# Optimization experiments

Measured on AMD Instinct MI355X. Metric: run time of the kernel, lower is better.

The kernel has to match this reference:

```python
import jax, jax.numpy as jnp
import numpy as np

D_PAIR = 128
D_BIAS = 128
N_HEAD = 4
D_HID = 32
B = 1
L = 384
EPS = 1e-5


def _layernorm(x, gamma, beta):
    m = jnp.mean(x, axis=-1, keepdims=True)
    v = jnp.var(x, axis=-1, keepdims=True)
    return (x - m) * jax.lax.rsqrt(v + EPS) * gamma + beta


def setup_inputs() -> dict:
    key = jax.random.key(0)
    ks = jax.random.split(key, 10)
    hd = N_HEAD * D_HID
    s = 0.02
    return {
        "pair": jax.random.normal(ks[0], (B, L, L, D_PAIR), jnp.float32),
        "bias": jax.random.normal(ks[1], (B, L, L, D_BIAS), jnp.float32),
        "gamma_p": jnp.ones((D_PAIR,), jnp.float32),
        "beta_p": jnp.zeros((D_PAIR,), jnp.float32),
        "gamma_b": jnp.ones((D_BIAS,), jnp.float32),
        "beta_b": jnp.zeros((D_BIAS,), jnp.float32),
        "Wq": jax.random.normal(ks[2], (D_PAIR, hd), jnp.float32) * s,
        "Wk": jax.random.normal(ks[3], (D_PAIR, hd), jnp.float32) * s,
        "Wv": jax.random.normal(ks[4], (D_PAIR, hd), jnp.float32) * s,
        "Wb": jax.random.normal(ks[5], (D_BIAS, N_HEAD), jnp.float32) * s,
        "Wg": jax.random.normal(ks[6], (D_PAIR, hd), jnp.float32) * s,
        "bg": jnp.ones((hd,), jnp.float32),
        "Wout": jax.random.normal(ks[7], (hd, D_PAIR), jnp.float32) * s,
        "bout": jnp.zeros((D_PAIR,), jnp.float32),
    }


def reference(pair, bias, gamma_p, beta_p, gamma_b, beta_b,
              Wq, Wk, Wv, Wb, Wg, bg, Wout, bout):
    h = Wb.shape[1]
    d = Wq.shape[1] // h
    Bn, Ln = pair.shape[:2]
    scaling = 1.0 / jnp.sqrt(jnp.asarray(d, pair.dtype))

    # is_row=True: attend along rows -> swap the two L axes
    pair_t = jnp.transpose(pair, (0, 2, 1, 3))
    bias_t = jnp.transpose(bias, (0, 2, 1, 3))

    pn = _layernorm(pair_t, gamma_p, beta_p)                     # [B,L,L,dp]
    q = (pn @ Wq).reshape(Bn, Ln, Ln, h, d) * scaling            # [B,n,i,h,d]
    k = (pn @ Wk).reshape(Bn, Ln, Ln, h, d) / Ln                 # [B,n,j,h,d]

    # mean-over-n biased axial attention logits: [B,i,j,h]
    attn = jnp.einsum('bnihk,bnjhk->bijh', q, k)
    attn = attn + _layernorm(bias_t, gamma_b, beta_b) @ Wb       # learned bias
    a = jax.nn.softmax(attn, axis=-2)                            # over j

    v = (pn @ Wv).reshape(Bn, Ln, Ln, h, d)                      # [B,n,j,h,d]
    o = jnp.einsum('bijh,bnjhd->bnihd', a, v).reshape(Bn, Ln, Ln, h * d)

    gate = jax.nn.sigmoid(pn @ Wg + bg)                          # [B,L,L,h*d]
    out = (gate * o) @ Wout + bout                               # [B,L,L,dp]

    return jnp.transpose(out, (0, 2, 1, 3))                      # undo is_row permute
```

## Files before the change

kernel.cpp:

```cpp
#include <hip/hip_runtime.h>

typedef unsigned short u16;
typedef unsigned int   u32;
typedef __attribute__((ext_vector_type(8))) short bf16x8;
typedef __attribute__((ext_vector_type(4))) float f32x4;

#define LL 384
#define DP 128
#define SZROW ((size_t)LL * LL)

#define SWZ(row, col) (((row) << 7) + (((((col) >> 3) ^ ((row) & 7)) << 3) | ((col) & 7)))

__device__ __forceinline__ u16 f2bf(float x) {
  u32 u = __builtin_bit_cast(u32, x);
  u = (u + 0x7FFFu + ((u >> 16) & 1u)) >> 16;
  return (u16)u;
}
__device__ __forceinline__ float bf2f(u16 h) {
  return __builtin_bit_cast(float, ((u32)h) << 16);
}
__device__ __forceinline__ uint2 pack4(float a, float b, float c, float d) {
  uint2 p;
  p.x = (u32)f2bf(a) | ((u32)f2bf(b) << 16);
  p.y = (u32)f2bf(c) | ((u32)f2bf(d) << 16);
  return p;
}


__global__ void k_prep(const float* __restrict__ Wq, const float* __restrict__ Wk,
                       const float* __restrict__ Wv, const float* __restrict__ Wg,
                       const float* __restrict__ Wout, u16* __restrict__ wbf) {
  int r = blockIdx.x, c = threadIdx.x, m = blockIdx.y;
  const float* W;
  float s = 1.0f;
  if (m == 0)      { W = Wq;  s = 0.17677669529663687f; }
  else if (m == 1) { W = Wk;  s = 1.0f / 384.0f; }
  else if (m == 2) { W = Wv; }
  else if (m == 3) { W = Wg; }
  else             { W = Wout; }
  wbf[m * DP * DP + r * DP + c] = f2bf(W[c * DP + r] * s);
}

template <int NS>
__device__ __forceinline__ void wave_gemm(const u16* __restrict__ W, const u16* pnl,
                                          int wave, int q, int r, f32x4 (&acc)[2][NS]) {
  const f32x4 FZ = {0.f, 0.f, 0.f, 0.f};
#pragma unroll
  for (int ms = 0; ms < 2; ++ms)
#pragma unroll
    for (int ns = 0; ns < NS; ++ns) acc[ms][ns] = FZ;
#pragma unroll
  for (int kc = 0; kc < 4; ++kc) {
    bf16x8 a0 = *(const bf16x8*)(W + (wave * 32 + r) * DP + kc * 32 + q * 8);
    bf16x8 a1 = *(const bf16x8*)(W + (wave * 32 + 16 + r) * DP + kc * 32 + q * 8);
#pragma unroll
    for (int ns = 0; ns < NS; ++ns) {
      bf16x8 b = *(const bf16x8*)(pnl + SWZ(ns * 16 + r, kc * 32 + q * 8));
      acc[0][ns] = __builtin_amdgcn_mfma_f32_16x16x32_bf16(a0, b, acc[0][ns], 0, 0, 0);
      acc[1][ns] = __builtin_amdgcn_mfma_f32_16x16x32_bf16(a1, b, acc[1][ns], 0, 0, 0);
    }
  }
}

__device__ __forceinline__ void wave_gemm_t(const u16* __restrict__ W, const u16* pnl,
                                            int wave, int q, int r, f32x4 (&acc)[8]) {
  const f32x4 FZ = {0.f, 0.f, 0.f, 0.f};
#pragma unroll
  for (int cb = 0; cb < 8; ++cb) acc[cb] = FZ;
#pragma unroll
  for (int kc = 0; kc < 4; ++kc) {
    bf16x8 a = *(const bf16x8*)(pnl + SWZ(wave * 16 + r, kc * 32 + q * 8));
#pragma unroll
    for (int cb = 0; cb < 8; ++cb) {
      bf16x8 b = *(const bf16x8*)(W + (cb * 16 + r) * DP + kc * 32 + q * 8);
      acc[cb] = __builtin_amdgcn_mfma_f32_16x16x32_bf16(a, b, acc[cb], 0, 0, 0);
    }
  }
}

__global__ __launch_bounds__(256) void k1_ln_proj(
    const float* __restrict__ pair, const float* __restrict__ gamma_p,
    const float* __restrict__ beta_p, const u16* __restrict__ wbf,
    const float* __restrict__ bg, u16* __restrict__ Qb, u16* __restrict__ Kb,
    u16* __restrict__ Vp, u16* __restrict__ Gtb) {
  __shared__ u16 pn[64 * 128];
  const int ib = blockIdx.x, n = blockIdx.y;
  const int tid = threadIdx.x;
  const int lane = tid & 63, wave = tid >> 6;
  const int q = lane >> 4, r = lane & 15;
  const int sub = lane & 15, rw = lane >> 4;
  const int c0 = sub * 8;
  const float4 gmA = *(const float4*)(gamma_p + c0);
  const float4 gmB = *(const float4*)(gamma_p + c0 + 4);
  const float4 btA = *(const float4*)(beta_p + c0);
  const float4 btB = *(const float4*)(beta_p + c0 + 4);

#pragma unroll
  for (int it = 0; it < 4; ++it) {
    const int il = it * 16 + wave * 4 + rw;
    const float* rowp = pair + ((size_t)(ib * 64 + il) * LL + n) * DP + c0;
    float4 xa = *(const float4*)rowp;
    float4 xb = *(const float4*)(rowp + 4);
    float s1 = xa.x + xa.y + xa.z + xa.w + xb.x + xb.y + xb.z + xb.w;
    float s2 = xa.x * xa.x + xa.y * xa.y + xa.z * xa.z + xa.w * xa.w +
               xb.x * xb.x + xb.y * xb.y + xb.z * xb.z + xb.w * xb.w;
#pragma unroll
    for (int m = 8; m >= 1; m >>= 1) { s1 += __shfl_xor(s1, m); s2 += __shfl_xor(s2, m); }
    float mean = s1 * (1.0f / 128.0f);
    float rs = rsqrtf(s2 * (1.0f / 128.0f) - mean * mean + 1e-5f);
    uint4 pk;
    pk.x = (u32)f2bf((xa.x - mean) * rs * gmA.x + btA.x) |
           ((u32)f2bf((xa.y - mean) * rs * gmA.y + btA.y) << 16);
    pk.y = (u32)f2bf((xa.z - mean) * rs * gmA.z + btA.z) |
           ((u32)f2bf((xa.w - mean) * rs * gmA.w + btA.w) << 16);
    pk.z = (u32)f2bf((xb.x - mean) * rs * gmB.x + btB.x) |
           ((u32)f2bf((xb.y - mean) * rs * gmB.y + btB.y) << 16);
    pk.w = (u32)f2bf((xb.z - mean) * rs * gmB.z + btB.z) |
           ((u32)f2bf((xb.w - mean) * rs * gmB.w + btB.w) << 16);
    *(uint4*)(&pn[SWZ(il, c0)]) = pk;
  }
  __syncthreads();

  f32x4 acc[2][4];

  wave_gemm<4>(wbf, pn, wave, q, r, acc);
#pragma unroll
  for (int ms = 0; ms < 2; ++ms) {
#pragma unroll
    for (int ns = 0; ns < 4; ++ns) {
      size_t base = (((size_t)n * 4 + wave) * LL + ib * 64 + ns * 16 + r) * 32 + ms * 16 + q * 4;
      *(uint2*)(Qb + base) = pack4(acc[ms][ns][0], acc[ms][ns][1], acc[ms][ns][2], acc[ms][ns][3]);
    }
  }
  wave_gemm<4>(wbf + DP * DP, pn, wave, q, r, acc);
#pragma unroll
  for (int ms = 0; ms < 2; ++ms) {
#pragma unroll
    for (int ns = 0; ns < 4; ++ns) {
      size_t base = (((size_t)n * 4 + wave) * LL + ib * 64 + ns * 16 + r) * 32 + ms * 16 + q * 4;
      *(uint2*)(Kb + base) = pack4(acc[ms][ns][0], acc[ms][ns][1], acc[ms][ns][2], acc[ms][ns][3]);
    }
  }
  {
    f32x4 acc2[8];
    wave_gemm_t(wbf + 2 * DP * DP, pn, wave, q, r, acc2);
    const int il0 = wave * 16 + q * 4;
    u16* dst = Vp + ((size_t)n * 12 + ib * 2 + (il0 >> 5)) * (128 * 32) + (il0 & 31);
#pragma unroll
    for (int cb = 0; cb < 8; ++cb) {
      int c = cb * 16 + r;
      *(uint2*)(dst + c * 32) = pack4(acc2[cb][0], acc2[cb][1], acc2[cb][2], acc2[cb][3]);
    }
  }
  {
    f32x4 acc2[8];
    wave_gemm_t(wbf + 3 * DP * DP, pn, wave, q, r, acc2);
    const int il0 = wave * 16 + q * 4;
#pragma unroll
    for (int cb = 0; cb < 8; ++cb) {
      int c = cb * 16 + r;
      float bgc = bg[c];
      float g0 = 1.0f / (1.0f + __expf(-(acc2[cb][0] + bgc)));
      float g1 = 1.0f / (1.0f + __expf(-(acc2[cb][1] + bgc)));
      float g2 = 1.0f / (1.0f + __expf(-(acc2[cb][2] + bgc)));
      float g3 = 1.0f / (1.0f + __expf(-(acc2[cb][3] + bgc)));
      *(uint2*)(Gtb + ((size_t)n * DP + c) * LL + ib * 64 + il0) = pack4(g0, g1, g2, g3);
    }
  }
}

__global__ __launch_bounds__(256) void k2a_bias(
    const float* __restrict__ bias, const float* __restrict__ gamma_b,
    const float* __restrict__ beta_b, const float* __restrict__ Wb,
    float* __restrict__ part) {
  const int lane = threadIdx.x & 63, wave = threadIdx.x >> 6;
  const int sub = lane & 15, rw = lane >> 4;
  const int row = blockIdx.x * 16 + wave * 4 + rw;
  const int i = row % LL, j = row / LL;
  const int c0 = sub * 8;
  const float* src = bias + (size_t)row * DP + c0;
  float4 xa = *(const float4*)src;
  float4 xb = *(const float4*)(src + 4);
  float s1 = xa.x + xa.y + xa.z + xa.w + xb.x + xb.y + xb.z + xb.w;
  float s2 = xa.x * xa.x + xa.y * xa.y + xa.z * xa.z + xa.w * xa.w +
             xb.x * xb.x + xb.y * xb.y + xb.z * xb.z + xb.w * xb.w;
#pragma unroll
  for (int m = 8; m >= 1; m >>= 1) { s1 += __shfl_xor(s1, m); s2 += __shfl_xor(s2, m); }
  float mean = s1 * (1.0f / 128.0f);
  float rs = rsqrtf(s2 * (1.0f / 128.0f) - mean * mean + 1e-5f);
  const float4 gmA = *(const float4*)(gamma_b + c0);
  const float4 gmB = *(const float4*)(gamma_b + c0 + 4);
  const float4 btA = *(const float4*)(beta_b + c0);
  const float4 btB = *(const float4*)(beta_b + c0 + 4);
  float y[8];
  y[0] = (xa.x - mean) * rs * gmA.x + btA.x;
  y[1] = (xa.y - mean) * rs * gmA.y + btA.y;
  y[2] = (xa.z - mean) * rs * gmA.z + btA.z;
  y[3] = (xa.w - mean) * rs * gmA.w + btA.w;
  y[4] = (xb.x - mean) * rs * gmB.x + btB.x;
  y[5] = (xb.y - mean) * rs * gmB.y + btB.y;
  y[6] = (xb.z - mean) * rs * gmB.z + btB.z;
  y[7] = (xb.w - mean) * rs * gmB.w + btB.w;
  f32x4 pv = {0.f, 0.f, 0.f, 0.f};
#pragma unroll
  for (int k = 0; k < 8; ++k) pv += y[k] * *(const f32x4*)(Wb + (c0 + k) * 4);
#pragma unroll
  for (int m = 8; m >= 1; m >>= 1) {
    pv[0] += __shfl_xor(pv[0], m); pv[1] += __shfl_xor(pv[1], m);
    pv[2] += __shfl_xor(pv[2], m); pv[3] += __shfl_xor(pv[3], m);
  }
  if (sub == 0) {
    size_t o = (size_t)i * LL + j;
    part[(size_t)32 * SZROW + o] = pv[0];
    part[(size_t)33 * SZROW + o] = pv[1];
    part[(size_t)34 * SZROW + o] = pv[2];
    part[(size_t)35 * SZROW + o] = pv[3];
  }
}

__global__ __launch_bounds__(256) void k2b_qk(const u16* __restrict__ Qb,
                                              const u16* __restrict__ Kb,
                                              float* __restrict__ part) {
  const int it = blockIdx.y, jt = blockIdx.x >> 3, nc = blockIdx.x & 7;
  const int lane = threadIdx.x & 63, h = threadIdx.x >> 6;
  const int q = lane >> 4, r = lane & 15;
  const f32x4 FZ = {0.f, 0.f, 0.f, 0.f};
  f32x4 acc[3][3];
#pragma unroll
  for (int a = 0; a < 3; ++a)
#pragma unroll
    for (int b = 0; b < 3; ++b) acc[a][b] = FZ;
#pragma unroll 2
  for (int n = nc * 48; n < nc * 48 + 48; ++n) {
    const u16* Qp = Qb + (((size_t)n * 4 + h) * LL + it * 48 + r) * 32 + q * 8;
    const u16* Kp = Kb + (((size_t)n * 4 + h) * LL + jt * 48 + r) * 32 + q * 8;
    bf16x8 av[3], bv[3];
#pragma unroll
    for (int s = 0; s < 3; ++s) {
      av[s] = *(const bf16x8*)(Qp + s * 16 * 32);
      bv[s] = *(const bf16x8*)(Kp + s * 16 * 32);
    }
#pragma unroll
    for (int is = 0; is < 3; ++is)
#pragma unroll
      for (int js = 0; js < 3; ++js)
        acc[is][js] = __builtin_amdgcn_mfma_f32_16x16x32_bf16(av[is], bv[js], acc[is][js], 0, 0, 0);
  }
  float* dst = part + (size_t)(nc * 4 + h) * SZROW;
#pragma unroll
  for (int is = 0; is < 3; ++is)
#pragma unroll
    for (int js = 0; js < 3; ++js)
#pragma unroll
      for (int reg = 0; reg < 4; ++reg)
        dst[(size_t)(it * 48 + is * 16 + q * 4 + reg) * LL + jt * 48 + js * 16 + r] =
            acc[is][js][reg];
}

__global__ __launch_bounds__(384) void k3_softmax(const float* __restrict__ part,
                                                  u16* __restrict__ ap) {
  const int i = blockIdx.x, h = blockIdx.y, j = threadIdx.x;
  __shared__ float red[6];
  float l = 0.f;
#pragma unroll
  for (int c = 0; c < 9; ++c) l += part[(size_t)(c * 4 + h) * SZROW + (size_t)i * LL + j];
  float m = l;
#pragma unroll
  for (int s = 32; s >= 1; s >>= 1) m = fmaxf(m, __shfl_xor(m, s));
  const int wv = threadIdx.x >> 6;
  if ((threadIdx.x & 63) == 0) red[wv] = m;
  __syncthreads();
  m = fmaxf(fmaxf(fmaxf(red[0], red[1]), fmaxf(red[2], red[3])), fmaxf(red[4], red[5]));
  float e = __expf(l - m);
  float s = e;
#pragma unroll
  for (int t = 32; t >= 1; t >>= 1) s += __shfl_xor(s, t);
  __syncthreads();
  if ((threadIdx.x & 63) == 0) red[wv] = s;
  __syncthreads();
  s = red[0] + red[1] + red[2] + red[3] + red[4] + red[5];
  ap[(((size_t)h * 12 + (j >> 5)) * LL + i) * 32 + (j & 31)] = f2bf(e / s);
}

__global__ __launch_bounds__(256) void k4_out(
    const u16* __restrict__ ap, const u16* __restrict__ Vp,
    const u16* __restrict__ Gtb, const u16* __restrict__ Wot,
    const float* __restrict__ bout, float* __restrict__ out) {
  __shared__ __align__(16) char smem[64 * 132 * 4];
  u16*   go = (u16*)smem;
  float* O  = (float*)smem;
  const int n = blockIdx.x, ib = blockIdx.y;
  const int tid = threadIdx.x;
  const int lane = tid & 63, wave = tid >> 6;
  const int h = wave;
  const int q = lane >> 4, r = lane & 15;

  uint2 gp[4][2];
#pragma unroll
  for (int is = 0; is < 4; ++is)
#pragma unroll
    for (int ds = 0; ds < 2; ++ds) {
      int c = h * 32 + ds * 16 + r;
      gp[is][ds] =
          *(const uint2*)(Gtb + ((size_t)n * DP + c) * LL + ib * 64 + is * 16 + q * 4);
    }

  const f32x4 FZ = {0.f, 0.f, 0.f, 0.f};
  f32x4 acc[4][2];
#pragma unroll
  for (int is = 0; is < 4; ++is) { acc[is][0] = FZ; acc[is][1] = FZ; }

  const u16* Vbase = Vp + (size_t)n * 12 * (128 * 32) + (h * 32 + r) * 32 + q * 8;
  const u16* Abase = ap + ((size_t)h * 12 * LL + ib * 64 + r) * 32 + q * 8;

  bf16x8 av[2][4];
#pragma unroll
  for (int is = 0; is < 4; ++is) av[0][is] = *(const bf16x8*)(Abase + (size_t)is * 16 * 32);

#pragma unroll
  for (int halfk = 0; halfk < 2; ++halfk) {
    bf16x8 vb[6][2];
#pragma unroll
    for (int k2 = 0; k2 < 6; ++k2) {
      const u16* Vkc = Vbase + (size_t)(halfk * 6 + k2) * (128 * 32);
      vb[k2][0] = *(const bf16x8*)(Vkc);
      vb[k2][1] = *(const bf16x8*)(Vkc + 16 * 32);
    }
#pragma unroll
    for (int k2 = 0; k2 < 6; ++k2) {
      const int kc = halfk * 6 + k2;
      const int cur = kc & 1, nxt = cur ^ 1;
      if (kc < 11) {
        const u16* An = Abase + (size_t)(kc + 1) * LL * 32;
#pragma unroll
        for (int is = 0; is < 4; ++is) av[nxt][is] = *(const bf16x8*)(An + (size_t)is * 16 * 32);
      }
#pragma unroll
      for (int is = 0; is < 4; ++is) {
        acc[is][0] = __builtin_amdgcn_mfma_f32_16x16x32_bf16(av[cur][is], vb[k2][0], acc[is][0], 0, 0, 0);
        acc[is][1] = __builtin_amdgcn_mfma_f32_16x16x32_bf16(av[cur][is], vb[k2][1], acc[is][1], 0, 0, 0);
      }
    }
  }
#pragma unroll
  for (int is = 0; is < 4; ++is)
#pragma unroll
    for (int ds = 0; ds < 2; ++ds) {
      int c = h * 32 + ds * 16 + r;
      float g0 = bf2f((u16)(gp[is][ds].x & 0xffff)), g1 = bf2f((u16)(gp[is][ds].x >> 16));
      float g2 = bf2f((u16)(gp[is][ds].y & 0xffff)), g3 = bf2f((u16)(gp[is][ds].y >> 16));
      int il = is * 16 + q * 4;
      go[SWZ(il + 0, c)] = f2bf(g0 * acc[is][ds][0]);
      go[SWZ(il + 1, c)] = f2bf(g1 * acc[is][ds][1]);
      go[SWZ(il + 2, c)] = f2bf(g2 * acc[is][ds][2]);
      go[SWZ(il + 3, c)] = f2bf(g3 * acc[is][ds][3]);
    }
  __syncthreads();

  f32x4 acc2[2][4];
  wave_gemm<4>(Wot, go, wave, q, r, acc2);
  __syncthreads();

#pragma unroll
  for (int ms = 0; ms < 2; ++ms) {
    int co = wave * 32 + ms * 16 + q * 4;
    f32x4 bo = *(const f32x4*)(bout + co);
#pragma unroll
    for (int ns = 0; ns < 4; ++ns)
      *(f32x4*)(O + (ns * 16 + r) * 132 + co) = acc2[ms][ns] + bo;
  }
  __syncthreads();
#pragma unroll
  for (int e = 0; e < 8; ++e) {
    int m = e * 256 + tid;
    int il = m >> 5, cw = (m & 31) * 4;
    *(f32x4*)(out + ((size_t)(ib * 64 + il) * LL + n) * DP + cw) =
        *(const f32x4*)(O + il * 132 + cw);
  }
}

extern "C" void kernel_launch(void* const* d_in, const int* in_sizes, int n_in,
                              void* d_out, int out_size, void* d_ws, size_t ws_size,
                              hipStream_t stream) {
  const float* pair    = (const float*)d_in[0];
  const float* bias    = (const float*)d_in[1];
  const float* gamma_p = (const float*)d_in[2];
  const float* beta_p  = (const float*)d_in[3];
  const float* gamma_b = (const float*)d_in[4];
  const float* beta_b  = (const float*)d_in[5];
  const float* Wq      = (const float*)d_in[6];
  const float* Wk      = (const float*)d_in[7];
  const float* Wv      = (const float*)d_in[8];
  const float* Wb      = (const float*)d_in[9];
  const float* Wg      = (const float*)d_in[10];
  const float* bg      = (const float*)d_in[11];
  const float* Wout    = (const float*)d_in[12];
  const float* bout    = (const float*)d_in[13];

  u16* Qb = (u16*)d_out;
  u16* Kb = Qb + (size_t)LL * LL * DP;

  char* ws = (char*)d_ws;
  const size_t BF_PLANE = (size_t)LL * LL * DP * 2;
  u16*   Vp   = (u16*)ws;
  u16*   Gtb  = (u16*)(ws + BF_PLANE);
  float* part = (float*)(ws + 2 * BF_PLANE);
  u16*   ap   = (u16*)(ws + 2 * BF_PLANE + 36 * SZROW * 4);
  u16*   wbf  = (u16*)(ws + 2 * BF_PLANE + 36 * SZROW * 4 + 4 * SZROW * 2);
  float* out  = (float*)d_out;

  k_prep<<<dim3(128, 5), 128, 0, stream>>>(Wq, Wk, Wv, Wg, Wout, wbf);
  k1_ln_proj<<<dim3(6, 384), 256, 0, stream>>>(pair, gamma_p, beta_p, wbf, bg, Qb, Kb, Vp, Gtb);
  k2a_bias<<<dim3(9216), 256, 0, stream>>>(bias, gamma_b, beta_b, Wb, part);
  k2b_qk<<<dim3(64, 8), 256, 0, stream>>>(Qb, Kb, part);
  k3_softmax<<<dim3(384, 4), 384, 0, stream>>>(part, ap);
  k4_out<<<dim3(384, 6), 256, 0, stream>>>(ap, Vp, Gtb, wbf + 4 * DP * DP, bout, out);
}
```

Measured before the change: 445.2 us.

## Stage V/gate outputs through LDS for coalesced stores; split n-reduction in QK kernel

In the LN+projection kernel, the V and gate projections now reuse the standard wave_gemm and write results into a padded shared-memory tile. They are then stored to the transposed global layouts as full 16-byte coalesced rows instead of scattered 8-byte writes. All pair loads are also issued before the layernorm math, so their latency overlaps. The QK logits kernel doubles its block to 512 threads, with two wave groups each reducing half of the n range using register double-buffered loads, then combining partial sums through LDS. This buys more parallelism and latency hiding at the cost of extra shared memory and barriers.

```diff
diff --git a/kernel.cpp b/kernel.cpp
--- a/kernel.cpp
+++ b/kernel.cpp
@@ -62,28 +62,13 @@
   }
 }
 
-__device__ __forceinline__ void wave_gemm_t(const u16* __restrict__ W, const u16* pnl,
-                                            int wave, int q, int r, f32x4 (&acc)[8]) {
-  const f32x4 FZ = {0.f, 0.f, 0.f, 0.f};
-#pragma unroll
-  for (int cb = 0; cb < 8; ++cb) acc[cb] = FZ;
-#pragma unroll
-  for (int kc = 0; kc < 4; ++kc) {
-    bf16x8 a = *(const bf16x8*)(pnl + SWZ(wave * 16 + r, kc * 32 + q * 8));
-#pragma unroll
-    for (int cb = 0; cb < 8; ++cb) {
-      bf16x8 b = *(const bf16x8*)(W + (cb * 16 + r) * DP + kc * 32 + q * 8);
-      acc[cb] = __builtin_amdgcn_mfma_f32_16x16x32_bf16(a, b, acc[cb], 0, 0, 0);
-    }
-  }
-}
-
 __global__ __launch_bounds__(256) void k1_ln_proj(
     const float* __restrict__ pair, const float* __restrict__ gamma_p,
     const float* __restrict__ beta_p, const u16* __restrict__ wbf,
     const float* __restrict__ bg, u16* __restrict__ Qb, u16* __restrict__ Kb,
     u16* __restrict__ Vp, u16* __restrict__ Gtb) {
   __shared__ u16 pn[64 * 128];
+  __shared__ u16 T[128 * 72];
   const int ib = blockIdx.x, n = blockIdx.y;
   const int tid = threadIdx.x;
   const int lane = tid & 63, wave = tid >> 6;
@@ -95,28 +80,35 @@
   const float4 btA = *(const float4*)(beta_p + c0);
   const float4 btB = *(const float4*)(beta_p + c0 + 4);
 
+  float4 xa[4], xb[4];
 #pragma unroll
   for (int it = 0; it < 4; ++it) {
     const int il = it * 16 + wave * 4 + rw;
     const float* rowp = pair + ((size_t)(ib * 64 + il) * LL + n) * DP + c0;
-    float4 xa = *(const float4*)rowp;
-    float4 xb = *(const float4*)(rowp + 4);
-    float s1 = xa.x + xa.y + xa.z + xa.w + xb.x + xb.y + xb.z + xb.w;
-    float s2 = xa.x * xa.x + xa.y * xa.y + xa.z * xa.z + xa.w * xa.w +
-               xb.x * xb.x + xb.y * xb.y + xb.z * xb.z + xb.w * xb.w;
+    xa[it] = *(const float4*)rowp;
+    xb[it] = *(const float4*)(rowp + 4);
+  }
+#pragma unroll
+  for (int it = 0; it < 4; ++it) {
+    const int il = it * 16 + wave * 4 + rw;
+    float s1 = xa[it].x + xa[it].y + xa[it].z + xa[it].w +
+               xb[it].x + xb[it].y + xb[it].z + xb[it].w;
+    float s2 = xa[it].x * xa[it].x + xa[it].y * xa[it].y + xa[it].z * xa[it].z +
+               xa[it].w * xa[it].w + xb[it].x * xb[it].x + xb[it].y * xb[it].y +
+               xb[it].z * xb[it].z + xb[it].w * xb[it].w;
 #pragma unroll
     for (int m = 8; m >= 1; m >>= 1) { s1 += __shfl_xor(s1, m); s2 += __shfl_xor(s2, m); }
     float mean = s1 * (1.0f / 128.0f);
     float rs = rsqrtf(s2 * (1.0f / 128.0f) - mean * mean + 1e-5f);
     uint4 pk;
-    pk.x = (u32)f2bf((xa.x - mean) * rs * gmA.x + btA.x) |
-           ((u32)f2bf((xa.y - mean) * rs * gmA.y + btA.y) << 16);
-    pk.y = (u32)f2bf((xa.z - mean) * rs * gmA.z + btA.z) |
-           ((u32)f2bf((xa.w - mean) * rs * gmA.w + btA.w) << 16);
-    pk.z = (u32)f2bf((xb.x - mean) * rs * gmB.x + btB.x) |
-           ((u32)f2bf((xb.y - mean) * rs * gmB.y + btB.y) << 16);
-    pk.w = (u32)f2bf((xb.z - mean) * rs * gmB.z + btB.z) |
-           ((u32)f2bf((xb.w - mean) * rs * gmB.w + btB.w) << 16);
+    pk.x = (u32)f2bf((xa[it].x - mean) * rs * gmA.x + btA.x) |
+           ((u32)f2bf((xa[it].y - mean) * rs * gmA.y + btA.y) << 16);
+    pk.y = (u32)f2bf((xa[it].z - mean) * rs * gmA.z + btA.z) |
+           ((u32)f2bf((xa[it].w - mean) * rs * gmA.w + btA.w) << 16);
+    pk.z = (u32)f2bf((xb[it].x - mean) * rs * gmB.x + btB.x) |
+           ((u32)f2bf((xb[it].y - mean) * rs * gmB.y + btB.y) << 16);
+    pk.w = (u32)f2bf((xb[it].z - mean) * rs * gmB.z + btB.z) |
+           ((u32)f2bf((xb[it].w - mean) * rs * gmB.w + btB.w) << 16);
     *(uint4*)(&pn[SWZ(il, c0)]) = pk;
   }
   __syncthreads();
@@ -141,31 +133,46 @@
       *(uint2*)(Kb + base) = pack4(acc[ms][ns][0], acc[ms][ns][1], acc[ms][ns][2], acc[ms][ns][3]);
     }
   }
-  {
-    f32x4 acc2[8];
-    wave_gemm_t(wbf + 2 * DP * DP, pn, wave, q, r, acc2);
-    const int il0 = wave * 16 + q * 4;
-    u16* dst = Vp + ((size_t)n * 12 + ib * 2 + (il0 >> 5)) * (128 * 32) + (il0 & 31);
-#pragma unroll
-    for (int cb = 0; cb < 8; ++cb) {
-      int c = cb * 16 + r;
-      *(uint2*)(dst + c * 32) = pack4(acc2[cb][0], acc2[cb][1], acc2[cb][2], acc2[cb][3]);
-    }
-  }
-  {
-    f32x4 acc2[8];
-    wave_gemm_t(wbf + 3 * DP * DP, pn, wave, q, r, acc2);
-    const int il0 = wave * 16 + q * 4;
-#pragma unroll
-    for (int cb = 0; cb < 8; ++cb) {
-      int c = cb * 16 + r;
-      float bgc = bg[c];
-      float g0 = 1.0f / (1.0f + __expf(-(acc2[cb][0] + bgc)));
-      float g1 = 1.0f / (1.0f + __expf(-(acc2[cb][1] + bgc)));
-      float g2 = 1.0f / (1.0f + __expf(-(acc2[cb][2] + bgc)));
-      float g3 = 1.0f / (1.0f + __expf(-(acc2[cb][3] + bgc)));
-      *(uint2*)(Gtb + ((size_t)n * DP + c) * LL + ib * 64 + il0) = pack4(g0, g1, g2, g3);
-    }
+  wave_gemm<4>(wbf + 2 * DP * DP, pn, wave, q, r, acc);
+#pragma unroll
+  for (int ms = 0; ms < 2; ++ms)
+#pragma unroll
+    for (int ns = 0; ns < 4; ++ns)
+#pragma unroll
+      for (int reg = 0; reg < 4; ++reg)
+        T[(wave * 32 + ms * 16 + q * 4 + reg) * 72 + ns * 16 + r] = f2bf(acc[ms][ns][reg]);
+  __syncthreads();
+#pragma unroll
+  for (int kk = 0; kk < 2; ++kk) {
+    u16* dst = Vp + ((size_t)n * 12 + ib * 2 + kk) * (128 * 32);
+#pragma unroll
+    for (int e = 0; e < 2; ++e) {
+      int m = e * 256 + tid;
+      int c = m >> 2, io = (m & 3) * 8;
+      *(uint4*)(dst + c * 32 + io) = *(const uint4*)(T + c * 72 + kk * 32 + io);
+    }
+  }
+  wave_gemm<4>(wbf + 3 * DP * DP, pn, wave, q, r, acc);
+  __syncthreads();
+#pragma unroll
+  for (int ms = 0; ms < 2; ++ms) {
+    f32x4 bgv = *(const f32x4*)(bg + wave * 32 + ms * 16 + q * 4);
+#pragma unroll
+    for (int ns = 0; ns < 4; ++ns)
+#pragma unroll
+      for (int reg = 0; reg < 4; ++reg) {
+        float x = acc[ms][ns][reg] + bgv[reg];
+        T[(wave * 32 + ms * 16 + q * 4 + reg) * 72 + ns * 16 + r] =
+            f2bf(1.0f / (1.0f + __expf(-x)));
+      }
+  }
+  __syncthreads();
+#pragma unroll
+  for (int it = 0; it < 4; ++it) {
+    int c = it * 32 + (tid >> 3);
+    int il2 = (tid & 7) * 8;
+    *(uint4*)(Gtb + ((size_t)n * DP + c) * LL + ib * 64 + il2) =
+        *(const uint4*)(T + c * 72 + il2);
   }
 }
 
@@ -218,11 +225,14 @@
   }
 }
 
-__global__ __launch_bounds__(256) void k2b_qk(const u16* __restrict__ Qb,
+__global__ __launch_bounds__(512) void k2b_qk(const u16* __restrict__ Qb,
                                               const u16* __restrict__ Kb,
                                               float* __restrict__ part) {
+  __shared__ f32x4 red[4][9][64];
   const int it = blockIdx.y, jt = blockIdx.x >> 3, nc = blockIdx.x & 7;
-  const int lane = threadIdx.x & 63, h = threadIdx.x >> 6;
+  const int tid = threadIdx.x;
+  const int lane = tid & 63, wave = tid >> 6;
+  const int h = wave & 3, nh = wave >> 2;
   const int q = lane >> 4, r = lane & 15;
   const f32x4 FZ = {0.f, 0.f, 0.f, 0.f};
   f32x4 acc[3][3];
@@ -230,31 +240,57 @@
   for (int a = 0; a < 3; ++a)
 #pragma unroll
     for (int b = 0; b < 3; ++b) acc[a][b] = FZ;
+
+  const int n0 = nc * 48 + nh * 24;
+  const size_t nstride = (size_t)4 * LL * 32;
+  const u16* Qp = Qb + (((size_t)n0 * 4 + h) * LL + it * 48 + r) * 32 + q * 8;
+  const u16* Kp = Kb + (((size_t)n0 * 4 + h) * LL + jt * 48 + r) * 32 + q * 8;
+
+  bf16x8 av[2][3], bv[2][3];
+#pragma unroll
+  for (int s = 0; s < 3; ++s) {
+    av[0][s] = *(const bf16x8*)(Qp + s * 16 * 32);
+    bv[0][s] = *(const bf16x8*)(Kp + s * 16 * 32);
+  }
 #pragma unroll 2
-  for (int n = nc * 48; n < nc * 48 + 48; ++n) {
-    const u16* Qp = Qb + (((size_t)n * 4 + h) * LL + it * 48 + r) * 32 + q * 8;
-    const u16* Kp = Kb + (((size_t)n * 4 + h) * LL + jt * 48 + r) * 32 + q * 8;
-    bf16x8 av[3], bv[3];
-#pragma unroll
-    for (int s = 0; s < 3; ++s) {
-      av[s] = *(const bf16x8*)(Qp + s * 16 * 32);
-      bv[s] = *(const bf16x8*)(Kp + s * 16 * 32);
+  for (int nn = 0; nn < 24; ++nn) {
+    const int cur = nn & 1, nxt = cur ^ 1;
+    if (nn < 23) {
+      const u16* Qn = Qp + (size_t)(nn + 1) * nstride;
+      const u16* Kn = Kp + (size_t)(nn + 1) * nstride;
+#pragma unroll
+      for (int s = 0; s < 3; ++s) {
+        av[nxt][s] = *(const bf16x8*)(Qn + s * 16 * 32);
+        bv[nxt][s] = *(const bf16x8*)(Kn + s * 16 * 32);
+      }
     }
 #pragma unroll
     for (int is = 0; is < 3; ++is)
 #pragma unroll
       for (int js = 0; js < 3; ++js)
-        acc[is][js] = __builtin_amdgcn_mfma_f32_16x16x32_bf16(av[is], bv[js], acc[is][js], 0, 0, 0);
-  }
-  float* dst = part + (size_t)(nc * 4 + h) * SZROW;
-#pragma unroll
-  for (int is = 0; is < 3; ++is)
-#pragma unroll
-    for (int js = 0; js < 3; ++js)
-#pragma unroll
-      for (int reg = 0; reg < 4; ++reg)
-        dst[(size_t)(it * 48 + is * 16 + q * 4 + reg) * LL + jt * 48 + js * 16 + r] =
-            acc[is][js][reg];
+        acc[is][js] =
+            __builtin_amdgcn_mfma_f32_16x16x32_bf16(av[cur][is], bv[cur][js], acc[is][js], 0, 0, 0);
+  }
+
+  if (nh == 1) {
+#pragma unroll
+    for (int is = 0; is < 3; ++is)
+#pragma unroll
+      for (int js = 0; js < 3; ++js) red[h][is * 3 + js][lane] = acc[is][js];
+  }
+  __syncthreads();
+  if (nh == 0) {
+    float* dst = part + (size_t)(nc * 4 + h) * SZROW;
+#pragma unroll
+    for (int is = 0; is < 3; ++is)
+#pragma unroll
+      for (int js = 0; js < 3; ++js) {
+        f32x4 v = acc[is][js] + red[h][is * 3 + js][lane];
+#pragma unroll
+        for (int reg = 0; reg < 4; ++reg)
+          dst[(size_t)(it * 48 + is * 16 + q * 4 + reg) * LL + jt * 48 + js * 16 + r] = v[reg];
+      }
+  }
 }
 
 __global__ __launch_bounds__(384) void k3_softmax(const float* __restrict__ part,
@@ -412,7 +448,7 @@
   k_prep<<<dim3(128, 5), 128, 0, stream>>>(Wq, Wk, Wv, Wg, Wout, wbf);
   k1_ln_proj<<<dim3(6, 384), 256, 0, stream>>>(pair, gamma_p, beta_p, wbf, bg, Qb, Kb, Vp, Gtb);
   k2a_bias<<<dim3(9216), 256, 0, stream>>>(bias, gamma_b, beta_b, Wb, part);
-  k2b_qk<<<dim3(64, 8), 256, 0, stream>>>(Qb, Kb, part);
+  k2b_qk<<<dim3(64, 8), 512, 0, stream>>>(Qb, Kb, part);
   k3_softmax<<<dim3(384, 4), 384, 0, stream>>>(part, ap);
   k4_out<<<dim3(384, 6), 256, 0, stream>>>(ap, Vp, Gtb, wbf + 4 * DP * DP, bout, out);
 }
```

Result: faster. 399.2 us (-10.3%).
